# Kernel tuning notes

Hardware: AMD Instinct MI355X
Metric: run time of the kernel (lower is better)

## Reference

```python
import jax, jax.numpy as jnp
import numpy as np

N_S, N_G, D, K = 30000, 3000, 128, 16
SIGMA = 2.5
BOX = 60.0  # Angstrom box for random coordinates


def setup_inputs() -> dict:
    key = jax.random.key(0)
    ks = jax.random.split(key, 10)
    s = 1.0 / np.sqrt(D)
    return {
        'xs': jax.random.normal(ks[0], (N_S, D), jnp.float32),
        'xg': jax.random.normal(ks[1], (N_G, D), jnp.float32),
        'pos_s': jax.random.uniform(ks[2], (N_S, 3), jnp.float32) * BOX,
        'pos_g': jax.random.uniform(ks[3], (N_G, 3), jnp.float32) * BOX,
        'W_s_pre': jax.random.normal(ks[4], (D, D), jnp.float32) * s,
        'W_g_pre': jax.random.normal(ks[5], (D, D), jnp.float32) * s,
        'W_gs': jax.random.normal(ks[6], (D, D), jnp.float32) * s,
        'W_sg': jax.random.normal(ks[7], (D, D), jnp.float32) * s,
        'W_s_post': jax.random.normal(ks[8], (2 * D, D), jnp.float32) * s,
        'W_g_post': jax.random.normal(ks[9], (2 * D, D), jnp.float32) * s,
        'k': K,
    }


def reference(xs, xg, pos_s, pos_g, W_s_pre, W_g_pre, W_gs, W_sg, W_s_post, W_g_post, k):
    n_s, d = xs.shape
    # ---- compute_bipartite_graphs: knn of each graph node over surface nodes ----
    # squared pairwise distances via gemm form: (N_G, N_S)
    d2 = ((pos_g ** 2).sum(-1)[:, None] + (pos_s ** 2).sum(-1)[None, :]
          - 2.0 * pos_g @ pos_s.T)
    neg_d2, idx = jax.lax.top_k(-d2, k)          # idx: (N_G, K) surface neighbors
    w = jnp.exp(neg_d2 / (2.0 * SIGMA ** 2))     # RBF edge weight exp(-d^2/(2*sigma^2))
    # ---- pre blocks ----
    hs = xs @ W_s_pre                             # (N_S, D)
    hg = xg @ W_g_pre                             # (N_G, D)
    # ---- bp_gs block: graph -> surface weighted edge-conv (scatter-add) ----
    msg_gs = (hg @ W_gs)[:, None, :] * w[:, :, None]          # (N_G, K, D)
    xs_out = jnp.zeros((n_s, d), hs.dtype).at[idx.reshape(-1)].add(
        msg_gs.reshape(-1, d))
    # ---- bp_sg block: surface -> graph weighted edge-conv (gather-sum) ----
    xg_out = ((hs @ W_sg)[idx] * w[:, :, None]).sum(axis=1)   # (N_G, D)
    # ---- post blocks: combine pre features with message output ----
    xs_new = jax.nn.relu(jnp.concatenate([hs, xs_out], axis=-1) @ W_s_post)
    xg_new = jax.nn.relu(jnp.concatenate([hg, xg_out], axis=-1) @ W_g_post)
    return xs_new, xg_new
```

## Files before the change

kernel.cpp:

```cpp
#include <hip/hip_runtime.h>
#include <stdint.h>

#define N_S 30000
#define N_G 3000
#define DD  128
#define KK  16
#define NE  (N_G * KK)
#define NC  16
#define CELLS (NC * NC * NC)
#define CH  3.75f
#define CAP 16
#define SURV 384
#define ECAP 32
#define EOVF_CAP 8192

#define FILL_BLOCKS 118
#define PACK_BLOCKS 384
#define NBS16 1875
#define NBG16 188
#define PRE_TILES (NBS16 + NBG16)
#define TASKS 5160
#define QBLOCKS 768
#define NWAVES (QBLOCKS * 4)
#define NBS 469
#define NBG 47
#define NTILE (NBS + NBG)

typedef unsigned long long ull;
#define INF_KEY 0x7F7FFFFF7FFFFFFFull

using v8s = __attribute__((ext_vector_type(8))) short;
using v4f = __attribute__((ext_vector_type(4))) float;

__device__ __forceinline__ float bf2f(unsigned short u) {
    union { unsigned int i; float f; } v; v.i = ((unsigned int)u) << 16; return v.f;
}
__device__ __forceinline__ unsigned short f2bf(float f) {
    union { float f; unsigned int i; } v; v.f = f;
    unsigned int x = v.i;
    return (unsigned short)((x + 0x7fffu + ((x >> 16) & 1u)) >> 16);
}
__device__ __forceinline__ float ldIn(const void* p, int i, int bf) {
    return bf ? bf2f(((const unsigned short*)p)[i]) : ((const float*)p)[i];
}
__device__ __forceinline__ void stOut(void* p, int i, float v, int bf) {
    if (bf) ((unsigned short*)p)[i] = f2bf(v);
    else    ((float*)p)[i] = v;
}
__device__ __forceinline__ int cellOf(float x) {
    int c = (int)(x * (1.0f / CH));
    if (c < 0) c = 0; if (c > NC - 1) c = NC - 1;
    return c;
}
__device__ __forceinline__ float dist2(float gx, float gy, float gz, float4 cd) {
    const float dx = gx - cd.x, dy = gy - cd.y, dz = gz - cd.z;
    return fmaf(dx, dx, fmaf(dy, dy, dz * dz));
}
__device__ __forceinline__ ull packKey(float d2, int sid) {
    return ((ull)__float_as_uint(d2) << 32) | (unsigned)sid;
}

__device__ __forceinline__ int detectFlag(const void* pos_g) {
    const unsigned int* w = (const unsigned int*)pos_g;
    int votes = 0;
#pragma unroll
    for (int i = 0; i < 16; ++i) {
        const unsigned int b = (w[i] >> 8) & 0xFFu;
        votes += (b >= 0x3Eu && b <= 0x42u) ? 1 : 0;
    }
    return votes >= 8;
}

__device__ __forceinline__ void emitEdge(int g, ull key, int rank,
                                         int* __restrict__ idx_out,
                                         float* __restrict__ w_out,
                                         int* __restrict__ scnt,
                                         int2* __restrict__ edge,
                                         int4* __restrict__ eovf,
                                         int* __restrict__ neovf)
{
    const int sid = (int)(unsigned)key;
    const float d2 = __uint_as_float((unsigned)(key >> 32));
    const float wv = expf(-d2 * (1.0f / 12.5f));
    idx_out[g * KK + rank] = sid;
    w_out[g * KK + rank] = wv;
    const int c = atomicAdd(&scnt[sid], 1);
    if (c < ECAP) {
        edge[(size_t)sid * ECAP + c] = make_int2(g, __float_as_int(wv));
    } else {
        const int o = atomicAdd(neovf, 1);
        if (o < EOVF_CAP) eovf[o] = make_int4(sid, g, __float_as_int(wv), 0);
    }
}

__device__ __forceinline__ void ins16(ull key, ull bk[KK]) {
    if (key >= bk[KK - 1]) return;
    ull c = key;
#pragma unroll
    for (int j = 0; j < KK; ++j) {
        const bool less = c < bk[j];
        const ull nk = less ? c : bk[j];
        const ull ok = less ? bk[j] : c;
        bk[j] = nk; c = ok;
    }
}

template<int R>
__device__ __forceinline__ float regionM2f(float gx, float gy, float gz,
                                           int cx, int cy, int cz)
{
    float m = 1e30f;
    if (cx - R > 0)      m = fminf(m, gx - (float)(cx - R) * CH);
    if (cx + R < NC - 1) m = fminf(m, (float)(cx + R + 1) * CH - gx);
    if (cy - R > 0)      m = fminf(m, gy - (float)(cy - R) * CH);
    if (cy + R < NC - 1) m = fminf(m, (float)(cy + R + 1) * CH - gy);
    if (cz - R > 0)      m = fminf(m, gz - (float)(cz - R) * CH);
    if (cz + R < NC - 1) m = fminf(m, (float)(cz + R + 1) * CH - gz);
    m = fmaxf(m, 0.f);
    return (m < 1e29f) ? m * m * (1.0f - 1e-5f) : 1e30f;
}

template<int R>
__device__ int scanR(int t, float gx, float gy, float gz,
                     int cx, int cy, int cz, float m2eff,
                     const int* __restrict__ ccnt,
                     const float4* __restrict__ scell,
                     const float4* __restrict__ ovf, int novf,
                     ull* __restrict__ skey)
{
    const int S = 2 * R + 1;
    const int S3 = S * S * S;
    int total = 0;

    for (int b0 = 0; b0 < 2 * S3; b0 += 64) {
        const int pt = b0 + t;
        int cnt = 0, base = 0;
        if (pt < 2 * S3) {
            const int cell = pt >> 1, h = pt & 1;
            const int dx = cell / (S * S) - R;
            const int dy = (cell / S) % S - R;
            const int dz = cell % S - R;
            const int X = cx + dx, Y = cy + dy, Z = cz + dz;
            if (X >= 0 && X < NC && Y >= 0 && Y < NC && Z >= 0 && Z < NC) {
                const int cid = (X * NC + Y) * NC + Z;
                int c = ccnt[cid]; if (c > CAP) c = CAP;
                const int lo = h * 8;
                const int hi = (c < lo + 8) ? c : (lo + 8);
                cnt = (hi > lo) ? (hi - lo) : 0;
                base = cid * CAP + lo;
            }
        }
        ull kv[8]; int okm = 0;
#pragma unroll
        for (int i = 0; i < 8; ++i) {
            kv[i] = 0;
            if (i < cnt) {
                const float4 cd = scell[base + i];
                const float d2 = dist2(gx, gy, gz, cd);
                if (d2 < m2eff) { okm |= (1 << i); kv[i] = packKey(d2, __float_as_int(cd.w)); }
            }
        }
        int myc = __popc(okm);
        int incl = myc;
        for (int d = 1; d < 64; d <<= 1) {
            int v = __shfl_up(incl, d);
            if (t >= d) incl += v;
        }
        int pos = total + (incl - myc);
        total += __shfl(incl, 63);
#pragma unroll
        for (int i = 0; i < 8; ++i) {
            if (okm & (1 << i)) {
                if (pos < SURV) skey[pos] = kv[i];
                ++pos;
            }
        }
        if (total > SURV) return total;
    }

    for (int i0 = 0; i0 < novf; i0 += 64) {
        const int i = i0 + t;
        bool act = (i < novf);
        ull key = 0;
        if (act) {
            const float4 cd = ovf[i];
            const float d2 = dist2(gx, gy, gz, cd);
            act = (d2 < m2eff);
            if (act) key = packKey(d2, __float_as_int(cd.w));
        }
        const ull b = __ballot(act);
        const int p2 = total + (int)__popcll(b & ((1ull << t) - 1ull));
        if (act && p2 < SURV) skey[p2] = key;
        total += (int)__popcll(b);
    }
    return total;
}

template<int NV>
__device__ void rankEmit(int t, int n, const ull* __restrict__ skey, int g,
                         int* __restrict__ idx_out, float* __restrict__ w_out,
                         int* __restrict__ scnt, int2* __restrict__ edge,
                         int4* __restrict__ eovf, int* __restrict__ neovf)
{
    asm volatile("s_waitcnt lgkmcnt(0)" ::: "memory");
    ull ki[NV]; int rk[NV]; int nv = 0;
    for (int i = t; i < n && nv < NV; i += 64) { ki[nv] = skey[i]; rk[nv] = 0; ++nv; }
    for (int j = 0; j < n; ++j) {
        const ull kj = skey[j];
#pragma unroll
        for (int q = 0; q < NV; ++q)
            if (q < nv) rk[q] += (kj < ki[q]) ? 1 : 0;
    }
#pragma unroll
    for (int q = 0; q < NV; ++q)
        if (q < nv && rk[q] < KK)
            emitEdge(g, ki[q], rk[q], idx_out, w_out, scnt, edge, eovf, neovf);
}

__attribute__((noinline))
__device__ void knn_brute(int g, int t, int bf,
                          const void* pos_g, const void* pos_s,
                          int* __restrict__ idx_out, float* __restrict__ w_out,
                          int* __restrict__ scnt, int2* __restrict__ edge,
                          int4* __restrict__ eovf, int* __restrict__ neovf)
{
    const float gx = ldIn(pos_g, 3 * g + 0, bf);
    const float gy = ldIn(pos_g, 3 * g + 1, bf);
    const float gz = ldIn(pos_g, 3 * g + 2, bf);

    ull bk[KK];
#pragma unroll
    for (int j = 0; j < KK; ++j) bk[j] = INF_KEY;

    for (int i = t; i < N_S; i += 64) {
        const float dx = gx - ldIn(pos_s, 3 * i + 0, bf);
        const float dy = gy - ldIn(pos_s, 3 * i + 1, bf);
        const float dz = gz - ldIn(pos_s, 3 * i + 2, bf);
        const float d2 = fmaf(dx, dx, fmaf(dy, dy, dz * dz));
        ins16(packKey(d2, i), bk);
    }

    ull myKey = INF_KEY;
    for (int p = 0; p < KK; ++p) {
        ull key = bk[0];
        for (int d = 1; d < 64; d <<= 1) {
            const ull ok = __shfl_xor(key, d);
            if (ok < key) key = ok;
        }
        if (t == p) myKey = key;
        if (bk[0] == key) {
#pragma unroll
            for (int j = 0; j < KK - 1; ++j) bk[j] = bk[j + 1];
            bk[KK - 1] = INF_KEY;
        }
    }
    if (t < KK)
        emitEdge(g, myKey, t, idx_out, w_out, scnt, edge, eovf, neovf);
}

__device__ void knn_task(int g, int t, int bf,
                         const void* pos_g, const void* pos_s,
                         const int* __restrict__ ccnt,
                         const float4* __restrict__ scell,
                         const float4* __restrict__ ovf, int novf,
                         int* __restrict__ idx, float* __restrict__ w,
                         int* __restrict__ scnt, int2* __restrict__ edge,
                         int4* __restrict__ eovf, int* __restrict__ neovf,
                         ull* __restrict__ skey)
{
    const float gx = ldIn(pos_g, 3 * g + 0, bf);
    const float gy = ldIn(pos_g, 3 * g + 1, bf);
    const float gz = ldIn(pos_g, 3 * g + 2, bf);
    const int cx = cellOf(gx), cy = cellOf(gy), cz = cellOf(gz);

    int total = scanR<1>(t, gx, gy, gz, cx, cy, cz,
                         regionM2f<1>(gx, gy, gz, cx, cy, cz),
                         ccnt, scell, ovf, novf, skey);
    if (total < KK)
        total = scanR<2>(t, gx, gy, gz, cx, cy, cz,
                         regionM2f<2>(gx, gy, gz, cx, cy, cz),
                         ccnt, scell, ovf, novf, skey);

    if (total >= KK && total <= SURV) {
        if (total <= 192)
            rankEmit<3>(t, total, skey, g, idx, w, scnt, edge, eovf, neovf);
        else
            rankEmit<6>(t, total, skey, g, idx, w, scnt, edge, eovf, neovf);
    } else {
        knn_brute(g, t, bf, pos_g, pos_s, idx, w, scnt, edge, eovf, neovf);
    }
}

__device__ __forceinline__ v8s loadA_bf16(const unsigned short* p) {
    return *(const v8s*)p;
}
__device__ __forceinline__ v8s loadA_f32v(const float* f) {
    const float4 a = *(const float4*)f;
    const float4 b = *(const float4*)(f + 4);
    v8s r;
    r[0] = (short)f2bf(a.x); r[1] = (short)f2bf(a.y);
    r[2] = (short)f2bf(a.z); r[3] = (short)f2bf(a.w);
    r[4] = (short)f2bf(b.x); r[5] = (short)f2bf(b.y);
    r[6] = (short)f2bf(b.z); r[7] = (short)f2bf(b.w);
    return r;
}
__device__ __forceinline__ v8s loadA_raw(const void* A, size_t off, int bf) {
    if (bf) return loadA_bf16((const unsigned short*)A + off);
    return loadA_f32v((const float*)A + off);
}

__device__ void pre_tile16(int task, int lane, int bf, const void* xs, const void* xg,
                           const unsigned short* __restrict__ wpk_ps,
                           const unsigned short* __restrict__ wpk_pg,
                           unsigned short* __restrict__ hsb,
                           unsigned short* __restrict__ hgb)
{
    const void* A; const unsigned short* wpk; unsigned short* outp; int M, m0;
    const bool is_s = (task < NBS16);
    if (is_s) { A = xs; wpk = wpk_ps; outp = hsb; M = N_S; m0 = task * 16; }
    else      { A = xg; wpk = wpk_pg; outp = hgb; M = N_G; m0 = (task - NBS16) * 16; }

    const int q = lane >> 4, lm = lane & 15;
    const int mrow = m0 + lm;
    const bool valid = (mrow < M);

    v4f acc[8];
#pragma unroll
    for (int t = 0; t < 8; ++t) acc[t] = {0.f, 0.f, 0.f, 0.f};
    for (int ks = 0; ks < 4; ++ks) {
        v8s a = {0,0,0,0,0,0,0,0};
        if (valid) a = loadA_raw(A, (size_t)mrow * 128 + ks * 32 + q * 8, bf);
        const unsigned short* wb = wpk + (size_t)(ks * 4 + q) * 128 * 8;
#pragma unroll
        for (int t = 0; t < 8; ++t) {
            const v8s bfr = *(const v8s*)(wb + (t * 16 + lm) * 8);
            acc[t] = __builtin_amdgcn_mfma_f32_16x16x32_bf16(a, bfr, acc[t], 0, 0, 0);
        }
    }
#pragma unroll
    for (int t = 0; t < 8; ++t)
#pragma unroll
        for (int r = 0; r < 4; ++r) {
            const int row = m0 + q * 4 + r;
            if (row < M) outp[(size_t)row * 128 + t * 16 + lm] = f2bf(acc[t][r]);
        }
}

__device__ void post_tile(int task, int bf,
                          const unsigned short* __restrict__ hsb,
                          const unsigned short* __restrict__ hgb,
                          const int* __restrict__ scnt,
                          const int2* __restrict__ edge,
                          const int4* __restrict__ eovf, int nov2,
                          const int* __restrict__ idx, const float* __restrict__ w,
                          const unsigned short* __restrict__ wpk_cs,
                          const unsigned short* __restrict__ wpk_cg,
                          void* out)
{
    const unsigned short* A1; const unsigned short* wpk;
    int M, m0, ooff;
    const bool is_s = (task < NBS);
    if (is_s) { A1 = hsb; wpk = wpk_cs; M = N_S; m0 = task * 64; ooff = 0; }
    else      { A1 = hgb; wpk = wpk_cg; M = N_G; m0 = (task - NBS) * 64; ooff = N_S * DD; }

    const int wave = threadIdx.x >> 6, lane = threadIdx.x & 63;
    const int q = lane >> 4, lm = lane & 15;
    const int mb = m0 + wave * 16;
    const int mrow = mb + lm;
    const bool valid = (mrow < M);

    v8s a2[4];
    if (valid) {
        float f[4][8];
#pragma unroll
        for (int si = 0; si < 4; ++si)
#pragma unroll
            for (int j = 0; j < 8; ++j) f[si][j] = 0.f;
        if (is_s) {
            const int c = scnt[mrow];
            const int cc = (c < ECAP) ? c : ECAP;
            for (int e = 0; e < cc; ++e) {
                const int2 ed = edge[(size_t)mrow * ECAP + e];
                const float we = __int_as_float(ed.y);
                const unsigned short* hrow = hgb + (size_t)ed.x * 128 + q * 8;
#pragma unroll
                for (int si = 0; si < 4; ++si) {
                    const v8s hv = *(const v8s*)(hrow + si * 32);
#pragma unroll
                    for (int j = 0; j < 8; ++j)
                        f[si][j] += we * bf2f((unsigned short)hv[j]);
                }
            }
            if (c > ECAP) {
                for (int e = 0; e < nov2; ++e) {
                    const int4 ov = eovf[e];
                    if (ov.x == mrow) {
                        const float we = __int_as_float(ov.z);
                        const unsigned short* hrow = hgb + (size_t)ov.y * 128 + q * 8;
#pragma unroll
                        for (int si = 0; si < 4; ++si) {
                            const v8s hv = *(const v8s*)(hrow + si * 32);
#pragma unroll
                            for (int j = 0; j < 8; ++j)
                                f[si][j] += we * bf2f((unsigned short)hv[j]);
                        }
                    }
                }
            }
        } else {
            for (int e = 0; e < KK; ++e) {
                const int gi = idx[mrow * KK + e];
                const float we = w[mrow * KK + e];
                const unsigned short* hrow = hsb + (size_t)gi * 128 + q * 8;
#pragma unroll
                for (int si = 0; si < 4; ++si) {
                    const v8s hv = *(const v8s*)(hrow + si * 32);
#pragma unroll
                    for (int j = 0; j < 8; ++j)
                        f[si][j] += we * bf2f((unsigned short)hv[j]);
                }
            }
        }
#pragma unroll
        for (int si = 0; si < 4; ++si) {
            v8s r;
#pragma unroll
            for (int j = 0; j < 8; ++j) r[j] = (short)f2bf(f[si][j]);
            a2[si] = r;
        }
    } else {
#pragma unroll
        for (int si = 0; si < 4; ++si) a2[si] = (v8s){0,0,0,0,0,0,0,0};
    }

    v4f acc[8];
#pragma unroll
    for (int t = 0; t < 8; ++t) acc[t] = {0.f, 0.f, 0.f, 0.f};
#pragma unroll
    for (int ks = 0; ks < 8; ++ks) {
        const int kk = ks * 32 + q * 8;
        v8s a;
        if (ks < 4) {
            a = (v8s){0,0,0,0,0,0,0,0};
            if (valid) a = loadA_bf16(A1 + (size_t)mrow * 128 + kk);
        } else {
            a = a2[ks - 4];
        }
        const unsigned short* wb = wpk + (size_t)(ks * 4 + q) * 128 * 8;
#pragma unroll
        for (int t = 0; t < 8; ++t) {
            const v8s bfr = *(const v8s*)(wb + (t * 16 + lm) * 8);
            acc[t] = __builtin_amdgcn_mfma_f32_16x16x32_bf16(a, bfr, acc[t], 0, 0, 0);
        }
    }
#pragma unroll
    for (int t = 0; t < 8; ++t)
#pragma unroll
        for (int r = 0; r < 4; ++r) {
            const int row = mb + q * 4 + r;
            if (row < M) {
                float v = acc[t][r];
                if (v < 0.f) v = 0.f;
                stOut(out, ooff + row * DD + t * 16 + lm, v, bf);
            }
        }
}

__global__ __launch_bounds__(256) void fill_pack_kernel(
    const void* pos_s, const void* pos_g,
    const void* Wsp, const void* Wgp, const void* Wgs, const void* Wsg,
    const void* Wspost, const void* Wgpost,
    int* __restrict__ ccnt, float4* __restrict__ scell,
    float4* __restrict__ ovf, int* __restrict__ novf,
    unsigned short* __restrict__ wpk_ps, unsigned short* __restrict__ wpk_pg,
    unsigned short* __restrict__ wpk_cs, unsigned short* __restrict__ wpk_cg)
{
    const int bf = detectFlag(pos_g);
    const int bid = blockIdx.x, tid = threadIdx.x;
    if (bid < FILL_BLOCKS) {
        const int p = bid * 256 + tid;
        if (p < N_S) {
            const float x = ldIn(pos_s, 3 * p + 0, bf);
            const float y = ldIn(pos_s, 3 * p + 1, bf);
            const float z = ldIn(pos_s, 3 * p + 2, bf);
            const int cid = (cellOf(x) * NC + cellOf(y)) * NC + cellOf(z);
            const int slot = atomicAdd(&ccnt[cid], 1);
            const float4 pt = make_float4(x, y, z, __int_as_float(p));
            if (slot < CAP) scell[cid * CAP + slot] = pt;
            else            ovf[atomicAdd(novf, 1)] = pt;
        }
        return;
    }
    __shared__ float rows[256];
    const int rt = bid - FILL_BLOCKS;
    const int half = tid >> 7, j = tid & 127;
    const int task = rt * 2 + half;
    float v; unsigned short* dst; int k;
    if (task < 128) { k = task; v = ldIn(Wsp, k * DD + j, bf); dst = wpk_ps; }
    else if (task < 256) { k = task - 128; v = ldIn(Wgp, k * DD + j, bf); dst = wpk_pg; }
    else {
        const int which_g = (task >= 512);
        const int r = which_g ? (task - 512) : (task - 256);
        const void* W1 = which_g ? Wsg : Wgs;
        const void* Wp = which_g ? Wgpost : Wspost;
        dst = which_g ? wpk_cg : wpk_cs;
        k = r;
        if (r < 128) v = ldIn(Wp, r * DD + j, bf);
        else {
            rows[half * 128 + j] = ldIn(W1, (r - 128) * DD + j, bf);
            __syncthreads();
            float acc = 0.f;
            for (int m = 0; m < DD; ++m)
                acc += rows[half * 128 + m] * ldIn(Wp, (DD + m) * DD + j, bf);
            v = acc;
        }
    }
    const int ks = k >> 5, q = (k >> 3) & 3, i = k & 7;
    dst[((ks * 4 + q) * 128 + j) * 8 + i] = f2bf(v);
}

__global__ __launch_bounds__(256) void knn_pre_kernel(
    const void* xs, const void* xg, const void* pos_s, const void* pos_g,
    const int* __restrict__ ccnt, const float4* __restrict__ scell,
    const float4* __restrict__ ovf, const int* __restrict__ novf,
    int* __restrict__ idx, float* __restrict__ w,
    int* __restrict__ scnt, int2* __restrict__ edge,
    int4* __restrict__ eovf, int* __restrict__ neovf,
    const unsigned short* __restrict__ wpk_ps,
    const unsigned short* __restrict__ wpk_pg,
    unsigned short* __restrict__ hsb, unsigned short* __restrict__ hgb)
{
    __shared__ ull skey[4][SURV];
    const int bf = detectFlag(pos_g);
    const int wv = threadIdx.x >> 6, lane = threadIdx.x & 63;
    const int nov = *novf;
    const int wid = blockIdx.x * 4 + wv;

    for (int t0 = wid; t0 < TASKS; t0 += NWAVES) {
        const int grp = t0 / 5, off = t0 - grp * 5;
        if (off < 3) {
            const int g = grp * 3 + off;
            if (g < N_G)
                knn_task(g, lane, bf, pos_g, pos_s, ccnt, scell, ovf, nov,
                         idx, w, scnt, edge, eovf, neovf, skey[wv]);
        } else {
            const int task = grp * 2 + (off - 3);
            if (task < PRE_TILES)
                pre_tile16(task, lane, bf, xs, xg, wpk_ps, wpk_pg, hsb, hgb);
        }
    }
}

__global__ __launch_bounds__(256) void mfma_post_kernel(
    const void* pos_g,
    const unsigned short* __restrict__ hsb, const unsigned short* __restrict__ hgb,
    const int* __restrict__ scnt, const int2* __restrict__ edge,
    const int4* __restrict__ eovf, const int* __restrict__ neovf,
    const int* __restrict__ idx, const float* __restrict__ w,
    const unsigned short* __restrict__ wpk_cs, const unsigned short* __restrict__ wpk_cg,
    void* out)
{
    const int bf = detectFlag(pos_g);
    int nov2 = *neovf; if (nov2 > EOVF_CAP) nov2 = EOVF_CAP;
    post_tile(blockIdx.x, bf, hsb, hgb, scnt, edge, eovf, nov2,
              idx, w, wpk_cs, wpk_cg, out);
}

extern "C" void kernel_launch(void* const* d_in, const int* in_sizes, int n_in,
                              void* d_out, int out_size, void* d_ws, size_t ws_size,
                              hipStream_t stream)
{
    const void* xs       = d_in[0];
    const void* xg       = d_in[1];
    const void* pos_s    = d_in[2];
    const void* pos_g    = d_in[3];
    const void* W_s_pre  = d_in[4];
    const void* W_g_pre  = d_in[5];
    const void* W_gs     = d_in[6];
    const void* W_sg     = d_in[7];
    const void* W_s_post = d_in[8];
    const void* W_g_post = d_in[9];
    (void)in_sizes; (void)n_in; (void)out_size; (void)ws_size;

    char* ws = (char*)d_ws;
    size_t off_b = 0;
    auto alloc = [&](size_t bytes) -> void* {
        void* p = ws + off_b;
        off_b = (off_b + bytes + 255) & ~((size_t)255);
        return p;
    };
    unsigned short* hsb    = (unsigned short*)alloc((size_t)N_S * DD * 2);
    unsigned short* hgb    = (unsigned short*)alloc((size_t)N_G * DD * 2);
    unsigned short* wpk_ps = (unsigned short*)alloc((size_t)DD * DD * 2);
    unsigned short* wpk_pg = (unsigned short*)alloc((size_t)DD * DD * 2);
    unsigned short* wpk_cs = (unsigned short*)alloc((size_t)2 * DD * DD * 2);
    unsigned short* wpk_cg = (unsigned short*)alloc((size_t)2 * DD * DD * 2);
    int*            idx    = (int*)   alloc((size_t)NE * 4);
    float*          w      = (float*) alloc((size_t)NE * 4);
    int*            ibase  = (int*)   alloc((size_t)(CELLS + 1 + N_S + 1) * 4);
    int*            ccnt   = ibase;
    int*            novf   = ibase + CELLS;
    int*            scnt   = ibase + CELLS + 1;
    int*            neovf  = ibase + CELLS + 1 + N_S;
    float4*         scell  = (float4*)alloc((size_t)CELLS * CAP * 16);
    float4*         ovf    = (float4*)alloc((size_t)N_S * 16);
    int2*           edge   = (int2*)  alloc((size_t)N_S * ECAP * 8);
    int4*           eovf   = (int4*)  alloc((size_t)EOVF_CAP * 16);

    hipMemsetAsync(ibase, 0, (size_t)(CELLS + 1 + N_S + 1) * 4, stream);

    fill_pack_kernel<<<FILL_BLOCKS + PACK_BLOCKS, 256, 0, stream>>>(
        pos_s, pos_g, W_s_pre, W_g_pre, W_gs, W_sg, W_s_post, W_g_post,
        ccnt, scell, ovf, novf, wpk_ps, wpk_pg, wpk_cs, wpk_cg);

    knn_pre_kernel<<<QBLOCKS, 256, 0, stream>>>(
        xs, xg, pos_s, pos_g, ccnt, scell, ovf, novf, idx, w,
        scnt, edge, eovf, neovf, wpk_ps, wpk_pg, hsb, hgb);

    mfma_post_kernel<<<NTILE, 256, 0, stream>>>(
        pos_g, hsb, hgb, scnt, edge, eovf, neovf, idx, w,
        wpk_cs, wpk_cg, d_out);
}
```

Measured before the change: 172.4 us.

## Split fused kernels, raise kNN grid size, vectorize gather index loads

Splits the combined fill/pack kernel into separate binning and weight-packing launches, and the post kernel into separate surface and graph launches. Raises the kNN/pre-block grid from 768 to 1024 blocks so more waves share the task list. Replaces the scalar per-edge idx/w loads in the graph-side gather with int4/float4 loads, unrolled four at a time. The extra launches add per-launch overhead and serialize work that previously shared one grid.

```diff
diff --git a/kernel.cpp b/kernel.cpp
--- a/kernel.cpp
+++ b/kernel.cpp
@@ -20,11 +20,10 @@
 #define NBG16 188
 #define PRE_TILES (NBS16 + NBG16)
 #define TASKS 5160
-#define QBLOCKS 768
+#define QBLOCKS 1024
 #define NWAVES (QBLOCKS * 4)
 #define NBS 469
 #define NBG 47
-#define NTILE (NBS + NBG)
 
 typedef unsigned long long ull;
 #define INF_KEY 0x7F7FFFFF7FFFFFFFull
@@ -408,16 +407,25 @@
                 }
             }
         } else {
-            for (int e = 0; e < KK; ++e) {
-                const int gi = idx[mrow * KK + e];
-                const float we = w[mrow * KK + e];
-                const unsigned short* hrow = hsb + (size_t)gi * 128 + q * 8;
-#pragma unroll
-                for (int si = 0; si < 4; ++si) {
-                    const v8s hv = *(const v8s*)(hrow + si * 32);
-#pragma unroll
-                    for (int j = 0; j < 8; ++j)
-                        f[si][j] += we * bf2f((unsigned short)hv[j]);
+            const int4*   ip = (const int4*)(idx + (size_t)mrow * KK);
+            const float4* wp = (const float4*)(w + (size_t)mrow * KK);
+#pragma unroll
+            for (int eb = 0; eb < 4; ++eb) {
+                const int4 i4 = ip[eb];
+                const float4 w4 = wp[eb];
+                const int   gis[4] = {i4.x, i4.y, i4.z, i4.w};
+                const float wes[4] = {w4.x, w4.y, w4.z, w4.w};
+#pragma unroll
+                for (int u = 0; u < 4; ++u) {
+                    const unsigned short* hrow = hsb + (size_t)gis[u] * 128 + q * 8;
+                    const float we = wes[u];
+#pragma unroll
+                    for (int si = 0; si < 4; ++si) {
+                        const v8s hv = *(const v8s*)(hrow + si * 32);
+#pragma unroll
+                        for (int j = 0; j < 8; ++j)
+                            f[si][j] += we * bf2f((unsigned short)hv[j]);
+                    }
                 }
             }
         }
@@ -466,35 +474,37 @@
         }
 }
 
-__global__ __launch_bounds__(256) void fill_pack_kernel(
+__global__ __launch_bounds__(256) void fill_bin_kernel(
     const void* pos_s, const void* pos_g,
+    int* __restrict__ ccnt, float4* __restrict__ scell,
+    float4* __restrict__ ovf, int* __restrict__ novf)
+{
+    const int bf = detectFlag(pos_g);
+    const int p = blockIdx.x * 256 + threadIdx.x;
+    if (p < N_S) {
+        const float x = ldIn(pos_s, 3 * p + 0, bf);
+        const float y = ldIn(pos_s, 3 * p + 1, bf);
+        const float z = ldIn(pos_s, 3 * p + 2, bf);
+        const int cid = (cellOf(x) * NC + cellOf(y)) * NC + cellOf(z);
+        const int slot = atomicAdd(&ccnt[cid], 1);
+        const float4 pt = make_float4(x, y, z, __int_as_float(p));
+        if (slot < CAP) scell[cid * CAP + slot] = pt;
+        else            ovf[atomicAdd(novf, 1)] = pt;
+    }
+}
+
+__global__ __launch_bounds__(256) void pack_w_kernel(
+    const void* pos_g,
     const void* Wsp, const void* Wgp, const void* Wgs, const void* Wsg,
     const void* Wspost, const void* Wgpost,
-    int* __restrict__ ccnt, float4* __restrict__ scell,
-    float4* __restrict__ ovf, int* __restrict__ novf,
     unsigned short* __restrict__ wpk_ps, unsigned short* __restrict__ wpk_pg,
     unsigned short* __restrict__ wpk_cs, unsigned short* __restrict__ wpk_cg)
 {
     const int bf = detectFlag(pos_g);
-    const int bid = blockIdx.x, tid = threadIdx.x;
-    if (bid < FILL_BLOCKS) {
-        const int p = bid * 256 + tid;
-        if (p < N_S) {
-            const float x = ldIn(pos_s, 3 * p + 0, bf);
-            const float y = ldIn(pos_s, 3 * p + 1, bf);
-            const float z = ldIn(pos_s, 3 * p + 2, bf);
-            const int cid = (cellOf(x) * NC + cellOf(y)) * NC + cellOf(z);
-            const int slot = atomicAdd(&ccnt[cid], 1);
-            const float4 pt = make_float4(x, y, z, __int_as_float(p));
-            if (slot < CAP) scell[cid * CAP + slot] = pt;
-            else            ovf[atomicAdd(novf, 1)] = pt;
-        }
-        return;
-    }
+    const int tid = threadIdx.x;
     __shared__ float rows[256];
-    const int rt = bid - FILL_BLOCKS;
     const int half = tid >> 7, j = tid & 127;
-    const int task = rt * 2 + half;
+    const int task = blockIdx.x * 2 + half;
     float v; unsigned short* dst; int k;
     if (task < 128) { k = task; v = ldIn(Wsp, k * DD + j, bf); dst = wpk_ps; }
     else if (task < 256) { k = task - 128; v = ldIn(Wgp, k * DD + j, bf); dst = wpk_pg; }
@@ -551,7 +561,7 @@
     }
 }
 
-__global__ __launch_bounds__(256) void mfma_post_kernel(
+__global__ __launch_bounds__(256) void post_s_kernel(
     const void* pos_g,
     const unsigned short* __restrict__ hsb, const unsigned short* __restrict__ hgb,
     const int* __restrict__ scnt, const int2* __restrict__ edge,
@@ -563,6 +573,21 @@
     const int bf = detectFlag(pos_g);
     int nov2 = *neovf; if (nov2 > EOVF_CAP) nov2 = EOVF_CAP;
     post_tile(blockIdx.x, bf, hsb, hgb, scnt, edge, eovf, nov2,
+              idx, w, wpk_cs, wpk_cg, out);
+}
+
+__global__ __launch_bounds__(256) void post_g_kernel(
+    const void* pos_g,
+    const unsigned short* __restrict__ hsb, const unsigned short* __restrict__ hgb,
+    const int* __restrict__ scnt, const int2* __restrict__ edge,
+    const int4* __restrict__ eovf, const int* __restrict__ neovf,
+    const int* __restrict__ idx, const float* __restrict__ w,
+    const unsigned short* __restrict__ wpk_cs, const unsigned short* __restrict__ wpk_cg,
+    void* out)
+{
+    const int bf = detectFlag(pos_g);
+    int nov2 = *neovf; if (nov2 > EOVF_CAP) nov2 = EOVF_CAP;
+    post_tile(NBS + blockIdx.x, bf, hsb, hgb, scnt, edge, eovf, nov2,
               idx, w, wpk_cs, wpk_cg, out);
 }
 
@@ -609,15 +634,22 @@
 
     hipMemsetAsync(ibase, 0, (size_t)(CELLS + 1 + N_S + 1) * 4, stream);
 
-    fill_pack_kernel<<<FILL_BLOCKS + PACK_BLOCKS, 256, 0, stream>>>(
-        pos_s, pos_g, W_s_pre, W_g_pre, W_gs, W_sg, W_s_post, W_g_post,
-        ccnt, scell, ovf, novf, wpk_ps, wpk_pg, wpk_cs, wpk_cg);
+    fill_bin_kernel<<<FILL_BLOCKS, 256, 0, stream>>>(
+        pos_s, pos_g, ccnt, scell, ovf, novf);
+
+    pack_w_kernel<<<PACK_BLOCKS, 256, 0, stream>>>(
+        pos_g, W_s_pre, W_g_pre, W_gs, W_sg, W_s_post, W_g_post,
+        wpk_ps, wpk_pg, wpk_cs, wpk_cg);
 
     knn_pre_kernel<<<QBLOCKS, 256, 0, stream>>>(
         xs, xg, pos_s, pos_g, ccnt, scell, ovf, novf, idx, w,
         scnt, edge, eovf, neovf, wpk_ps, wpk_pg, hsb, hgb);
 
-    mfma_post_kernel<<<NTILE, 256, 0, stream>>>(
+    post_s_kernel<<<NBS, 256, 0, stream>>>(
         pos_g, hsb, hgb, scnt, edge, eovf, neovf, idx, w,
         wpk_cs, wpk_cg, d_out);
-}
+
+    post_g_kernel<<<NBG, 256, 0, stream>>>(
+        pos_g, hsb, hgb, scnt, edge, eovf, neovf, idx, w,
+        wpk_cs, wpk_cg, d_out);
+}
```

New measurement: 209.3 us. +21.4%, slower.
